# Optimization experiments

Hardware: AMD Instinct MI355X
Metric: run time of the kernel (lower is better)

The kernel has to match this reference:

```python
import jax, jax.numpy as jnp
import numpy as np


def setup_inputs() -> dict:
    key = jax.random.key(0)
    kx, ka, kb, kc = jax.random.split(key, 4)
    B, S = 32, 16384
    K, L, M = 4, 10, 10
    return {
        "x": jax.random.normal(kx, (B, S, 2), dtype=jnp.float32),
        "a": jax.random.normal(ka, (K, L), dtype=jnp.float32),
        "b": jax.random.normal(kb, (K, L, M), dtype=jnp.float32),
        "c": jax.random.normal(kc, (K, L, M), dtype=jnp.float32),  # unused in forward (matches original)
    }


def reference(x, a, b, c):
    # Generalized Memory Polynomial.
    # y[n] = sum_{k,l} a[k,l] * x[n-L+1+l] * |x[n-L+1+l]|^k
    #      + sum_{k,l,m} b[k,l,m] * x[n-l] * |x[n-l-(m+1)]|^(k+1), for n >= L+M, else 0.
    K, L = a.shape
    M = b.shape[2]
    B, S, _ = x.shape
    D = L + M  # max shift needed is (L-1)+M < D

    xc = x[..., 0] + 1j * x[..., 1]  # (B, S) complex64

    # Shifted views: xs[d][:, n] = x[:, n-d] (zero for n < d; masked out below anyway).
    xp = jnp.pad(xc, ((0, 0), (D - 1, 0)))
    xs = jnp.stack([xp[:, D - 1 - d: D - 1 - d + S] for d in range(D)])  # (D, B, S)

    absx = jnp.abs(xs)  # (D, B, S)
    # pows[k, d] = |x[n-d]|^k, k in 0..K
    pows = absx[None] ** jnp.arange(K + 1, dtype=x.dtype)[:, None, None, None]  # (K+1, D, B, S)

    # Term 1: shift d = L-1-l  ->  coefficient a[k, L-1-d]
    a_rev = a[:, ::-1]  # (K, L), a_rev[k, d] = a[k, L-1-d]
    coef1 = jnp.einsum('kd,kdbs->dbs', a_rev, pows[:K, :L])  # real (L, B, S)
    y = jnp.einsum('dbs,dbs->bs', coef1.astype(xc.dtype), xs[:L])  # complex (B, S)

    # Term 2: y += sum_{k,l,m} b[k,l,m] * x[n-l] * |x[n-l-m-1]|^(k+1)
    for l in range(L):  # small structural loop (L=10)
        coef2 = jnp.einsum('km,kmbs->bs', b[:, l, :], pows[1:, l + 1: l + 1 + M])  # real (B, S)
        y = y + coef2.astype(xc.dtype) * xs[l]

    # Only n >= L+M is written in the original (y initialized to zero elsewhere).
    mask = (jnp.arange(S) >= D).astype(x.dtype)  # (S,)
    y = y * mask

    out = jnp.stack([jnp.real(y), jnp.imag(y)], axis=-1)  # (B, S, 2)
    return out
```

## Files before the change

### kernel.cpp

```cpp
#include <hip/hip_runtime.h>


typedef short short8 __attribute__((ext_vector_type(8)));
typedef float f32x4 __attribute__((ext_vector_type(4)));

constexpr int S_FIXED = 16384;
constexpr int BLK = 256;
constexpr int TILE = 512;
constexpr int GROUPS = 9;
constexpr int QSN = 544;
constexpr int WLW = 148;

__device__ __forceinline__ unsigned short bfc(float f) {
    union { float f; unsigned u; } v; v.f = f;
    const unsigned u = v.u;
    return (unsigned short)((u + 0x7FFFu + ((u >> 16) & 1u)) >> 16);
}

__device__ __forceinline__ unsigned cvtpk(float lo, float hi) {
    unsigned r;
    asm("v_cvt_pk_bf16_f32 %0, %1, %2" : "=v"(r) : "v"(lo), "v"(hi));
    return r;
}

__device__ __forceinline__ short8 mk8(ushort4 lo, ushort4 hi) {
    union { ushort4 u[2]; short8 s; } x;
    x.u[0] = lo; x.u[1] = hi;
    return x.s;
}

__global__ __launch_bounds__(BLK) void gmp_mfma(
    const float* __restrict__ x,
    const float* __restrict__ a,
    const float* __restrict__ b,
    float* __restrict__ out,
    int S)
{
    __shared__ alignas(16) unsigned short th[16][64];
    __shared__ alignas(16) ushort4 qs[QSN];
    __shared__ alignas(16) float wl[4][10][WLW];

    const int t = threadIdx.x;
    const int wid = t >> 6, lane = t & 63;
    const int m = lane & 15, h = lane >> 4;
    const int blocksPerRow = S / TILE;
    const int brow = blockIdx.x / blocksPerRow;
    const int s0   = (blockIdx.x % blocksPerRow) * TILE;
    const int s0w  = s0 + 128 * wid;

    for (int idx = t; idx < 1024; idx += BLK) {
        const int col = idx >> 6, f = idx & 63;
        float v = 0.f;
        if (col < 10 && f < 44) {
            const int j = f >> 2, c = f & 3;
            if (j == 0) { if (c < 3) v = a[(c + 1) * 10 + (9 - col)]; }
            else v = b[c * 100 + col * 10 + (j - 1)];
        }
        th[col][f] = bfc(v);
    }

    const float2* __restrict__ xr2 =
        reinterpret_cast<const float2*>(x) + (size_t)brow * S;
    for (int i = t; i < QSN; i += BLK) {
        const int p = s0 + 515 - i;
        float xre = 0.f, xim = 0.f;
        if (p >= 0 && p < S) { const float2 v = xr2[p]; xre = v.x; xim = v.y; }
        const float m2 = xre * xre + xim * xim;
        const float r  = __builtin_amdgcn_sqrtf(m2);
        uint2 q;
        q.x = cvtpk(r, m2);
        q.y = cvtpk(m2 * r, m2 * m2);
        *reinterpret_cast<uint2*>(&qs[i]) = q;
    }
    __syncthreads();

    const short8 bfr0 = *reinterpret_cast<const short8*>(&th[m][8 * h]);
    const short8 bfr1 = *reinterpret_cast<const short8*>(&th[m][8 * h + 32]);

    const int ibase = 527 - 128 * wid;
    #pragma unroll
    for (int g = 0; g < GROUPS; ++g) {
        const int i1 = ibase - 16 * g - m + 2 * h;
        const short8 af0 = mk8(qs[i1],     qs[i1 + 1]);
        const short8 af1 = mk8(qs[i1 + 8], qs[i1 + 9]);
        f32x4 acc = {0.f, 0.f, 0.f, 0.f};
        acc = __builtin_amdgcn_mfma_f32_16x16x32_bf16(af0, bfr0, acc, 0, 0, 0);
        acc = __builtin_amdgcn_mfma_f32_16x16x32_bf16(af1, bfr1, acc, 0, 0, 0);
        if (m < 10)
            *reinterpret_cast<f32x4*>(&wl[wid][m][16 * g + 4 * h]) = acc;
    }

    const int sa0 = s0w + 2 * lane;
    const float4* __restrict__ xr4 =
        reinterpret_cast<const float4*>(x) + (size_t)brow * (S / 2);
    float xf[24];
    {
        const int base4 = (sa0 - 10) / 2;
        #pragma unroll
        for (int n = 0; n < 6; ++n) {
            int idx = base4 + n;
            if (idx < 0) idx = 0;
            const float4 f4 = xr4[idx];
            xf[4 * n + 0] = f4.x; xf[4 * n + 1] = f4.y;
            xf[4 * n + 2] = f4.z; xf[4 * n + 3] = f4.w;
        }
    }
    float yr0 = 0.f, yi0 = 0.f, yr1 = 0.f, yi1 = 0.f;
    #pragma unroll
    for (int l = 0; l < 10; ++l) {
        const float bl = a[9 - l];
        const float w0 = wl[wid][l][2 * lane + 12 - l] + bl;
        const float w1 = wl[wid][l][2 * lane + 13 - l] + bl;
        const int wp = 10 - l;
        yr0 += w0 * xf[2 * wp];     yi0 += w0 * xf[2 * wp + 1];
        yr1 += w1 * xf[2 * wp + 2]; yi1 += w1 * xf[2 * wp + 3];
    }
    const bool k0 = sa0 >= 20, k1 = (sa0 + 1) >= 20;
    const float4 o = make_float4(k0 ? yr0 : 0.f, k0 ? yi0 : 0.f,
                                 k1 ? yr1 : 0.f, k1 ? yi1 : 0.f);
    reinterpret_cast<float4*>(out)[((size_t)brow * S + sa0) / 2] = o;
}

extern "C" void kernel_launch(void* const* d_in, const int* in_sizes, int n_in,
                              void* d_out, int out_size, void* d_ws, size_t ws_size,
                              hipStream_t stream) {
    const float* x = (const float*)d_in[0];
    const float* a = (const float*)d_in[1];
    const float* b = (const float*)d_in[2];
    float* out = (float*)d_out;

    const int S = S_FIXED;
    const int B = in_sizes[0] / (2 * S);
    const int nblocks = B * (S / TILE);

    gmp_mfma<<<dim3(nblocks), dim3(BLK), 0, stream>>>(x, a, b, out, S);
}
```

Before: 11.11 us.

## Give each wave a private magnitude-power LDS window and issue x loads early

Replaces the shared block-wide table of packed |x| powers with a per-wave window of 160 entries, filled with float4 loads that produce two samples per lane. The per-wave x register loads used for the final accumulation are moved before the coefficient-table setup and the barrier, so their global-memory latency overlaps the LDS fills. This cuts the scalar loop over 544 entries and the latency exposed after the barrier, at the cost of some duplicated halo computation across waves and clamped out-of-range loads.

Measured after the change: 11.36 us. 1.02x slower.

```diff
diff --git a/kernel.cpp b/kernel.cpp
--- a/kernel.cpp
+++ b/kernel.cpp
@@ -8,7 +8,8 @@
 constexpr int BLK = 256;
 constexpr int TILE = 512;
 constexpr int GROUPS = 9;
-constexpr int QSN = 544;
+constexpr int IMAX = 143;
+constexpr int QRN = 160;
 constexpr int WLW = 148;
 
 __device__ __forceinline__ unsigned short bfc(float f) {
@@ -37,7 +38,7 @@
     int S)
 {
     __shared__ alignas(16) unsigned short th[16][64];
-    __shared__ alignas(16) ushort4 qs[QSN];
+    __shared__ alignas(16) ushort4 qr[4][QRN];
     __shared__ alignas(16) float wl[4][10][WLW];
 
     const int t = threadIdx.x;
@@ -47,6 +48,38 @@
     const int brow = blockIdx.x / blocksPerRow;
     const int s0   = (blockIdx.x % blocksPerRow) * TILE;
     const int s0w  = s0 + 128 * wid;
+    const int vb   = s0w - 12;
+
+    const float4* __restrict__ xr4 =
+        reinterpret_cast<const float4*>(x) + (size_t)brow * (S / 2);
+
+    const int sa0 = s0w + 2 * lane;
+    float xf[24];
+    {
+        const int base4 = (sa0 - 10) / 2;
+        #pragma unroll
+        for (int n = 0; n < 6; ++n) {
+            int idx = base4 + n;
+            if (idx < 0) idx = 0;
+            const float4 f4 = xr4[idx];
+            xf[4 * n + 0] = f4.x; xf[4 * n + 1] = f4.y;
+            xf[4 * n + 2] = f4.z; xf[4 * n + 3] = f4.w;
+        }
+    }
+
+    float4 qx0, qx1;
+    {
+        int i40 = (vb + 142 - 2 * lane) / 2;
+        if (i40 < 0) i40 = 0;
+        if (i40 > S / 2 - 1) i40 = S / 2 - 1;
+        qx0 = xr4[i40];
+        if (lane < 16) {
+            int i41 = (vb + 142 - 2 * (64 + lane)) / 2;
+            if (i41 < 0) i41 = 0;
+            if (i41 > S / 2 - 1) i41 = S / 2 - 1;
+            qx1 = xr4[i41];
+        }
+    }
 
     for (int idx = t; idx < 1024; idx += BLK) {
         const int col = idx >> 6, f = idx & 63;
@@ -59,30 +92,36 @@
         th[col][f] = bfc(v);
     }
 
-    const float2* __restrict__ xr2 =
-        reinterpret_cast<const float2*>(x) + (size_t)brow * S;
-    for (int i = t; i < QSN; i += BLK) {
-        const int p = s0 + 515 - i;
-        float xre = 0.f, xim = 0.f;
-        if (p >= 0 && p < S) { const float2 v = xr2[p]; xre = v.x; xim = v.y; }
-        const float m2 = xre * xre + xim * xim;
-        const float r  = __builtin_amdgcn_sqrtf(m2);
-        uint2 q;
-        q.x = cvtpk(r, m2);
-        q.y = cvtpk(m2 * r, m2 * m2);
-        *reinterpret_cast<uint2*>(&qs[i]) = q;
+    {
+        const float m2a = qx0.z * qx0.z + qx0.w * qx0.w;
+        const float ra  = __builtin_amdgcn_sqrtf(m2a);
+        const float m2b = qx0.x * qx0.x + qx0.y * qx0.y;
+        const float rb  = __builtin_amdgcn_sqrtf(m2b);
+        uint4 o;
+        o.x = cvtpk(ra, m2a);        o.y = cvtpk(m2a * ra, m2a * m2a);
+        o.z = cvtpk(rb, m2b);        o.w = cvtpk(m2b * rb, m2b * m2b);
+        *reinterpret_cast<uint4*>(&qr[wid][2 * lane]) = o;
+        if (lane < 16) {
+            const float m2c = qx1.z * qx1.z + qx1.w * qx1.w;
+            const float rc  = __builtin_amdgcn_sqrtf(m2c);
+            const float m2d = qx1.x * qx1.x + qx1.y * qx1.y;
+            const float rd  = __builtin_amdgcn_sqrtf(m2d);
+            uint4 o2;
+            o2.x = cvtpk(rc, m2c);   o2.y = cvtpk(m2c * rc, m2c * m2c);
+            o2.z = cvtpk(rd, m2d);   o2.w = cvtpk(m2d * rd, m2d * m2d);
+            *reinterpret_cast<uint4*>(&qr[wid][128 + 2 * lane]) = o2;
+        }
     }
     __syncthreads();
 
     const short8 bfr0 = *reinterpret_cast<const short8*>(&th[m][8 * h]);
     const short8 bfr1 = *reinterpret_cast<const short8*>(&th[m][8 * h + 32]);
 
-    const int ibase = 527 - 128 * wid;
     #pragma unroll
     for (int g = 0; g < GROUPS; ++g) {
-        const int i1 = ibase - 16 * g - m + 2 * h;
-        const short8 af0 = mk8(qs[i1],     qs[i1 + 1]);
-        const short8 af1 = mk8(qs[i1 + 8], qs[i1 + 9]);
+        const int i1 = IMAX - 16 * g - m + 2 * h;
+        const short8 af0 = mk8(qr[wid][i1],     qr[wid][i1 + 1]);
+        const short8 af1 = mk8(qr[wid][i1 + 8], qr[wid][i1 + 9]);
         f32x4 acc = {0.f, 0.f, 0.f, 0.f};
         acc = __builtin_amdgcn_mfma_f32_16x16x32_bf16(af0, bfr0, acc, 0, 0, 0);
         acc = __builtin_amdgcn_mfma_f32_16x16x32_bf16(af1, bfr1, acc, 0, 0, 0);
@@ -90,21 +129,6 @@
             *reinterpret_cast<f32x4*>(&wl[wid][m][16 * g + 4 * h]) = acc;
     }
 
-    const int sa0 = s0w + 2 * lane;
-    const float4* __restrict__ xr4 =
-        reinterpret_cast<const float4*>(x) + (size_t)brow * (S / 2);
-    float xf[24];
-    {
-        const int base4 = (sa0 - 10) / 2;
-        #pragma unroll
-        for (int n = 0; n < 6; ++n) {
-            int idx = base4 + n;
-            if (idx < 0) idx = 0;
-            const float4 f4 = xr4[idx];
-            xf[4 * n + 0] = f4.x; xf[4 * n + 1] = f4.y;
-            xf[4 * n + 2] = f4.z; xf[4 * n + 3] = f4.w;
-        }
-    }
     float yr0 = 0.f, yi0 = 0.f, yr1 = 0.f, yi1 = 0.f;
     #pragma unroll
     for (int l = 0; l < 10; ++l) {
```
